# Optimization experiments

Measured on AMD Instinct MI355X. Metric: run time of the kernel, lower is better.

## Reference

```python
import jax, jax.numpy as jnp
import numpy as np

B, S, C = 16, 720, 862      # batch, seq_len, enc_in
P = 24                      # highest_freq_period
PAD = 720                   # seq_len % P == 0 -> pad_len == seq_len (no padding branch taken)
LQ = PAD // P               # 30, per-branch subsequence length == conv channels
DM = 128                    # d_model (PECBlock hidden conv channels)
EL = 2                      # e_layers
PRED = 336                  # pred_len
EPS = 1e-5                  # RevIN eps


def setup_inputs() -> dict:
    key = jax.random.key(0)
    ks = jax.random.split(key, 6)
    x = jax.random.normal(ks[0], (B, S, C), jnp.float32)
    # per-layer, per-branch pointwise conv weights (kernel_size=1, no bias)
    W1 = jax.random.normal(ks[1], (EL, P, DM, LQ), jnp.float32) * 0.05   # conv1: LQ -> DM
    W2 = jax.random.normal(ks[2], (EL, P, LQ, DM), jnp.float32) * 0.05   # conv2: DM -> LQ
    proj_w = jax.random.normal(ks[3], (PRED, S), jnp.float32) * 0.02      # Linear(seq_len, pred_len)
    proj_b = jnp.zeros((PRED,), jnp.float32)
    rev_w = jnp.ones((C,), jnp.float32)    # RevIN affine weight
    rev_b = jnp.zeros((C,), jnp.float32)   # RevIN affine bias
    return dict(x=x, W1=W1, W2=W2, proj_w=proj_w, proj_b=proj_b, rev_w=rev_w, rev_b=rev_b)


def reference(x, W1, W2, proj_w, proj_b, rev_w, rev_b):
    # RevIN 'norm': stats over time dim (unbiased=False var), affine
    mean = jnp.mean(x, axis=1, keepdims=True)
    stdev = jnp.sqrt(jnp.var(x, axis=1, keepdims=True) + EPS)
    xn = (x - mean) / stdev * rev_w + rev_b

    # seq_len % P == 0 so pad_time_series is identity
    x_padded = xn
    # NOTE: original loop feeds x_padded into EVERY block (not chained),
    # so each iteration overwrites y; replicated faithfully.
    # Strided gather idx::P == reshape (B,C,LQ,P) and index last axis;
    # scatter reassembly y[:,:,idx::P]=... == reshape back from (B,C,LQ,P).
    xs = x_padded.transpose(0, 2, 1).reshape(B, C, LQ, P)  # (B,C,LQ,P)
    y = x_padded
    for l in range(EL):
        h = jax.nn.gelu(jnp.einsum('pdq,bcqp->pbdc', W1[l], xs), approximate=False)  # (P,B,DM,C)
        ys = jnp.einsum('pqd,pbdc->bcqp', W2[l], h)                                  # (B,C,LQ,P)
        y = ys.reshape(B, C, PAD).transpose(0, 2, 1)                                 # (B,PAD,C)

    # PredictedProjection: Linear over time dim
    out = jnp.einsum('ps,bsc->bpc', proj_w, y[:, :S, :]) + proj_b[None, :, None]  # (B,PRED,C)

    # RevIN 'denorm'
    out = (out - rev_b) / (rev_w + EPS * EPS)
    out = out * stdev + mean
    return out
```

## Files before the change

kernel.cpp:

```cpp
#include <hip/hip_runtime.h>
#include <math.h>

typedef __attribute__((ext_vector_type(8))) short bf16x8;
typedef __attribute__((ext_vector_type(4))) short short4v;
typedef __attribute__((ext_vector_type(4))) float f32x4;

#define NB 16
#define NS 720
#define NC 862
#define NP 24
#define NQ 30
#define NDM 128
#define NPRED 336
#define BC (NB*NC)
#define SCH 10
#define SLEN 72
#define KP 768
#define PBASE (4*BC)
#define WOFF_F (24*BC)

__device__ __forceinline__ short f2bf(float f) {
    union { float f; unsigned u; } v; v.f = f;
    unsigned r = v.u + 0x7FFFu + ((v.u >> 16) & 1u);
    return (short)(r >> 16);
}

__device__ __forceinline__ float gelu_f(float h) {
    float hc = fminf(fmaxf(h, -8.f), 8.f);
    float z2 = hc * hc;
    float zz = hc * (0.79788456f + 0.035677408f * z2);
    float e  = __expf(-2.f * zz);
    return h * __builtin_amdgcn_rcpf(1.f + e);
}

__global__ __launch_bounds__(256) void stats_partial_k(const float* __restrict__ x,
                                                       float* __restrict__ ws) {
    int b = blockIdx.x, ct = blockIdx.y, ch = blockIdx.z;
    int c = ct * 256 + threadIdx.x;
    if (c >= NC) return;
    const float* xp = x + ((size_t)b * NS + (size_t)ch * SLEN) * NC + c;
    float s = 0.f, sq = 0.f;
    #pragma unroll 4
    for (int i = 0; i < SLEN; ++i) {
        float v = xp[(size_t)i * NC];
        s += v; sq += v * v;
    }
    int idx = b * NC + c;
    float* ps = ws + PBASE;
    ps[(size_t)ch * BC + idx] = s;
    ps[(size_t)(SCH + ch) * BC + idx] = sq;
}

__global__ __launch_bounds__(256) void stats_final_k(float* __restrict__ ws,
                                                     const float* __restrict__ revw,
                                                     const float* __restrict__ revb) {
    int idx = blockIdx.x * 256 + threadIdx.x;
    if (idx >= BC) return;
    const float* ps = ws + PBASE;
    float s = 0.f, sq = 0.f;
    #pragma unroll
    for (int ch = 0; ch < SCH; ++ch) {
        s  += ps[(size_t)ch * BC + idx];
        sq += ps[(size_t)(SCH + ch) * BC + idx];
    }
    int c = idx % NC;
    float mean  = s * (1.f / NS);
    float var   = sq * (1.f / NS) - mean * mean;
    float stdev = sqrtf(var + 1e-5f);
    float rstd  = 1.f / stdev;
    float aw = revw[c] * rstd;
    float u  = stdev / (revw[c] + 1e-10f);
    ws[idx]          = aw;
    ws[BC + idx]     = revb[c] - mean * aw;
    ws[2 * BC + idx] = u;
    ws[3 * BC + idx] = mean - revb[c] * u;
}

__global__ __launch_bounds__(256) void wprep_k(const float* __restrict__ W1,
                                               const float* __restrict__ W2,
                                               unsigned short* __restrict__ W1FF,
                                               unsigned short* __restrict__ W2FF) {
    int p = blockIdx.x, tid = threadIdx.x;
    const float* w1 = W1 + (size_t)(NP + p) * NDM * NQ;
    const float* w2 = W2 + (size_t)(NP + p) * NQ * NDM;
    #pragma unroll
    for (int pass = 0; pass < 2; ++pass) {
        int s = pass * 256 + tid;
        int l = s & 63, lr = l & 15, lg = l >> 4;
        {
            int dt = s >> 6;
            int d = dt * 16 + lr;
            bf16x8 v;
            #pragma unroll
            for (int j = 0; j < 8; ++j) {
                int q = 8 * lg + j;
                v[j] = f2bf(q < NQ ? w1[d * NQ + q] : 0.f);
            }
            ((bf16x8*)(W1FF + (size_t)p * 4096))[s] = v;
        }
        {
            int g = s >> 6, mi = g >> 2, ks = g & 3;
            int q = mi * 16 + lr, k = ks * 32 + 8 * lg;
            bf16x8 v;
            #pragma unroll
            for (int j = 0; j < 8; ++j)
                v[j] = f2bf(q < NQ ? w2[q * NDM + k + j] : 0.f);
            ((bf16x8*)(W2FF + (size_t)p * 4096))[s] = v;
        }
    }
}

__global__ __launch_bounds__(256) void pwprep_k(const float* __restrict__ pw,
                                                unsigned short* __restrict__ PWPF) {
    int t = blockIdx.x * 256 + threadIdx.x;
    if (t >= 24 * 24 * 64) return;
    int l = t & 63, ks = (t >> 6) % 24, st = t / (24 * 64);
    int lr = l & 15, lg = l >> 4;
    int m = st * 16 + lr;
    bf16x8 v;
    #pragma unroll
    for (int j = 0; j < 8; ++j) {
        int q = 8 * lg + j;
        v[j] = f2bf((m < NPRED && q < NQ) ? pw[(size_t)m * NS + q * NP + ks] : 0.f);
    }
    ((bf16x8*)PWPF)[t] = v;
}

__global__ __launch_bounds__(256) void branch_k(const float* __restrict__ x,
        const unsigned short* __restrict__ W1FF, const unsigned short* __restrict__ W2FF,
        const float* __restrict__ ws, unsigned short* __restrict__ y_t) {
    __shared__ __align__(16) short XsB[4 * 64 * 8];
    __shared__ __align__(16) short HB [16 * 64 * 8];
    int tid = threadIdx.x;
    int c0 = blockIdx.x * 64;
    int p  = blockIdx.y;
    int b  = blockIdx.z;

    {
        int c  = tid & 63, kb = tid >> 6;
        int cg = c0 + c;
        bool cv = cg < NC;
        int ce = cv ? cg : NC - 1;
        float aw = ws[b * NC + ce];
        float bw = ws[BC + b * NC + ce];
        const float* xb = x + ((size_t)b * NS + p) * NC + ce;
        bf16x8 v;
        #pragma unroll
        for (int j = 0; j < 8; ++j) {
            int q = kb * 8 + j;
            float val = (q < NQ && cv) ? xb[(size_t)q * NP * NC] * aw + bw : 0.f;
            v[j] = f2bf(val);
        }
        *(bf16x8*)&XsB[(size_t)(kb * 64 + (c ^ kb)) * 8] = v;
    }

    int w = tid >> 6, l = tid & 63, lr = l & 15, lg = l >> 4;
    f32x4 zf = {0.f, 0.f, 0.f, 0.f};
    const bf16x8* w1p = (const bf16x8*)(W1FF + (size_t)p * 4096);
    const bf16x8* w2p = (const bf16x8*)(W2FF + (size_t)p * 4096);
    bf16x8 a0 = w1p[(2 * w) * 64 + l];
    bf16x8 a1 = w1p[(2 * w + 1) * 64 + l];

    __syncthreads();

    f32x4 hc[2][4];
    #pragma unroll
    for (int ni = 0; ni < 4; ++ni) {
        bf16x8 bfr = *(const bf16x8*)&XsB[(size_t)(lg * 64 + ((ni * 16 + lr) ^ lg)) * 8];
        hc[0][ni] = __builtin_amdgcn_mfma_f32_16x16x32_bf16(a0, bfr, zf, 0, 0, 0);
        hc[1][ni] = __builtin_amdgcn_mfma_f32_16x16x32_bf16(a1, bfr, zf, 0, 0, 0);
    }
    #pragma unroll
    for (int mi2 = 0; mi2 < 2; ++mi2) {
        int d0 = (2 * w + mi2) * 16 + 4 * lg;
        int kb = d0 >> 3, sub = d0 & 7;
        #pragma unroll
        for (int ni = 0; ni < 4; ++ni) {
            short4v v;
            #pragma unroll
            for (int r = 0; r < 4; ++r)
                v[r] = f2bf(gelu_f(hc[mi2][ni][r]));
            int col = ni * 16 + lr;
            *(short4v*)&HB[(size_t)(kb * 64 + (col ^ kb)) * 8 + sub] = v;
        }
    }
    __syncthreads();

    f32x4 yacc[2] = {zf, zf};
    #pragma unroll
    for (int ks = 0; ks < 4; ++ks) {
        int kb = ks * 4 + lg;
        bf16x8 hfr = *(const bf16x8*)&HB[(size_t)(kb * 64 + ((w * 16 + lr) ^ kb)) * 8];
        #pragma unroll
        for (int mi = 0; mi < 2; ++mi) {
            bf16x8 w2f = w2p[(mi * 4 + ks) * 64 + l];
            yacc[mi] = __builtin_amdgcn_mfma_f32_16x16x32_bf16(w2f, hfr, yacc[mi], 0, 0, 0);
        }
    }
    int cg2 = c0 + w * 16 + lr;
    if (cg2 < NC) {
        unsigned short* base = y_t + ((size_t)(b * NC + cg2)) * KP + p * 32;
        #pragma unroll
        for (int mi = 0; mi < 2; ++mi) {
            int q0 = mi * 16 + 4 * lg;
            short4v v;
            #pragma unroll
            for (int r = 0; r < 4; ++r)
                v[r] = (q0 + r < NQ) ? f2bf(yacc[mi][r]) : (short)0;
            *(short4v*)(base + q0) = v;
        }
    }
}

__global__ __launch_bounds__(256) void proj_k(const unsigned short* __restrict__ PWPF,
        const float* __restrict__ pb, const float* __restrict__ ws,
        const unsigned short* __restrict__ y_t, float* __restrict__ out) {
    int tid = threadIdx.x;
    int n0 = blockIdx.x * 128, m0 = blockIdx.y * 64, b = blockIdx.z;
    int w = tid >> 6, l = tid & 63, lr = l & 15, lg = l >> 4;
    int st0 = m0 >> 4;
    f32x4 zf = {0.f, 0.f, 0.f, 0.f};
    f32x4 acc[4][2];
    #pragma unroll
    for (int mi = 0; mi < 4; ++mi) { acc[mi][0] = zf; acc[mi][1] = zf; }

    const unsigned short* ytb = y_t + (size_t)b * NC * KP;
    int cA = n0 + 2 * w * 16 + lr;        if (cA > NC - 1) cA = NC - 1;
    int cB = n0 + (2 * w + 1) * 16 + lr;  if (cB > NC - 1) cB = NC - 1;
    const unsigned short* rowA = ytb + (size_t)cA * KP + lg * 8;
    const unsigned short* rowB = ytb + (size_t)cB * KP + lg * 8;
    const bf16x8* apb = (const bf16x8*)PWPF + (size_t)st0 * 24 * 64 + l;

    union u16x8 { uint4 u; bf16x8 v; };
    bf16x8 af0[4], af1[4];
    u16x8 b00, b01, b10, b11;

#define LOADF(AF, B0, B1, KS) do {                                   \
        AF[0] = apb[(0 * 24 + (KS)) * 64];                           \
        AF[1] = apb[(1 * 24 + (KS)) * 64];                           \
        AF[2] = apb[(2 * 24 + (KS)) * 64];                           \
        AF[3] = apb[(3 * 24 + (KS)) * 64];                           \
        B0.u = *(const uint4*)(rowA + (KS) * 32);                    \
        B1.u = *(const uint4*)(rowB + (KS) * 32); } while (0)
#define MM(AF, B0, B1) do {                                          \
        _Pragma("unroll")                                            \
        for (int mi = 0; mi < 4; ++mi) {                             \
            acc[mi][0] = __builtin_amdgcn_mfma_f32_16x16x32_bf16(AF[mi], B0.v, acc[mi][0], 0, 0, 0); \
            acc[mi][1] = __builtin_amdgcn_mfma_f32_16x16x32_bf16(AF[mi], B1.v, acc[mi][1], 0, 0, 0); \
        } } while (0)

    LOADF(af0, b00, b01, 0);
    #pragma unroll
    for (int ks = 0; ks < 24; ks += 2) {
        LOADF(af1, b10, b11, ks + 1);
        MM(af0, b00, b01);
        if (ks + 2 < 24) LOADF(af0, b00, b01, ks + 2);
        MM(af1, b10, b11);
    }
#undef LOADF
#undef MM

    #pragma unroll
    for (int mi = 0; mi < 4; ++mi) {
        #pragma unroll
        for (int r = 0; r < 4; ++r) {
            int pr = m0 + mi * 16 + 4 * lg + r;
            if (pr >= NPRED) continue;
            float bias = pb[pr];
            #pragma unroll
            for (int nj = 0; nj < 2; ++nj) {
                int c = n0 + (2 * w + nj) * 16 + lr;
                if (c >= NC) continue;
                int idx = b * NC + c;
                out[((size_t)b * NPRED + pr) * NC + c] =
                    (acc[mi][nj][r] + bias) * ws[2 * BC + idx] + ws[3 * BC + idx];
            }
        }
    }
}

extern "C" void kernel_launch(void* const* d_in, const int* in_sizes, int n_in,
                              void* d_out, int out_size, void* d_ws, size_t ws_size,
                              hipStream_t stream) {
    const float* x   = (const float*)d_in[0];
    const float* W1  = (const float*)d_in[1];
    const float* W2  = (const float*)d_in[2];
    const float* pw  = (const float*)d_in[3];
    const float* pb  = (const float*)d_in[4];
    const float* rw  = (const float*)d_in[5];
    const float* rb  = (const float*)d_in[6];
    float* out = (float*)d_out;
    float* ws  = (float*)d_ws;
    unsigned short* W1FF = (unsigned short*)(ws + WOFF_F);
    unsigned short* W2FF = W1FF + NP * 4096;
    unsigned short* PWPF = W2FF + NP * 4096;
    unsigned short* y_t  = PWPF + 24 * 24 * 64 * 8;

    stats_partial_k<<<dim3(NB, 4, SCH), 256, 0, stream>>>(x, ws);
    wprep_k<<<dim3(NP), 256, 0, stream>>>(W1, W2, W1FF, W2FF);
    pwprep_k<<<dim3((24 * 24 * 64 + 255) / 256), 256, 0, stream>>>(pw, PWPF);
    stats_final_k<<<dim3((BC + 255) / 256), 256, 0, stream>>>(ws, rw, rb);
    branch_k<<<dim3(14, NP, NB), 256, 0, stream>>>(x, W1FF, W2FF, ws, y_t);
    proj_k<<<dim3(7, 6, NB), 256, 0, stream>>>(PWPF, pb, ws, y_t, out);
}
```

Measured before the change: 93.62 us.

## Stage projection operands through LDS with async global-to-LDS loads and flatten columns

Rewrites proj_k so each wave loads one A tile and two B tiles per k-step straight into double-buffered shared memory via global_load_lds. The waves then read all four A fragments from LDS, so the A fragments are shared across waves instead of every wave loading them from global memory. The batch and channel dimensions are flattened into one column axis, which removes the per-batch tail waste of partially filled 128-column tiles. A __syncthreads per k-step and an integer division in the epilogue are added in exchange.

```diff
diff --git a/kernel.cpp b/kernel.cpp
--- a/kernel.cpp
+++ b/kernel.cpp
@@ -18,6 +18,7 @@
 #define KP 768
 #define PBASE (4*BC)
 #define WOFF_F (24*BC)
+#define NCOL (NB*NC)
 
 __device__ __forceinline__ short f2bf(float f) {
     union { float f; unsigned u; } v; v.f = f;
@@ -31,6 +32,12 @@
     float zz = hc * (0.79788456f + 0.035677408f * z2);
     float e  = __expf(-2.f * zz);
     return h * __builtin_amdgcn_rcpf(1.f + e);
+}
+
+__device__ __forceinline__ void gl_lds16(const void* g, void* l) {
+    __builtin_amdgcn_global_load_lds(
+        (const __attribute__((address_space(1))) unsigned int*)g,
+        (__attribute__((address_space(3))) unsigned int*)l, 16, 0, 0);
 }
 
 __global__ __launch_bounds__(256) void stats_partial_k(const float* __restrict__ x,
@@ -212,53 +219,49 @@
     }
 }
 
-__global__ __launch_bounds__(256) void proj_k(const unsigned short* __restrict__ PWPF,
+__global__ __launch_bounds__(256, 4) void proj_k(const unsigned short* __restrict__ PWPF,
         const float* __restrict__ pb, const float* __restrict__ ws,
         const unsigned short* __restrict__ y_t, float* __restrict__ out) {
+    __shared__ __align__(16) short L[2][12 * 512];
     int tid = threadIdx.x;
-    int n0 = blockIdx.x * 128, m0 = blockIdx.y * 64, b = blockIdx.z;
     int w = tid >> 6, l = tid & 63, lr = l & 15, lg = l >> 4;
-    int st0 = m0 >> 4;
+    int gn0 = blockIdx.x * 128;
+    int m0  = blockIdx.y * 64;
     f32x4 zf = {0.f, 0.f, 0.f, 0.f};
     f32x4 acc[4][2];
     #pragma unroll
     for (int mi = 0; mi < 4; ++mi) { acc[mi][0] = zf; acc[mi][1] = zf; }
 
-    const unsigned short* ytb = y_t + (size_t)b * NC * KP;
-    int cA = n0 + 2 * w * 16 + lr;        if (cA > NC - 1) cA = NC - 1;
-    int cB = n0 + (2 * w + 1) * 16 + lr;  if (cB > NC - 1) cB = NC - 1;
-    const unsigned short* rowA = ytb + (size_t)cA * KP + lg * 8;
-    const unsigned short* rowB = ytb + (size_t)cB * KP + lg * 8;
-    const bf16x8* apb = (const bf16x8*)PWPF + (size_t)st0 * 24 * 64 + l;
-
-    union u16x8 { uint4 u; bf16x8 v; };
-    bf16x8 af0[4], af1[4];
-    u16x8 b00, b01, b10, b11;
-
-#define LOADF(AF, B0, B1, KS) do {                                   \
-        AF[0] = apb[(0 * 24 + (KS)) * 64];                           \
-        AF[1] = apb[(1 * 24 + (KS)) * 64];                           \
-        AF[2] = apb[(2 * 24 + (KS)) * 64];                           \
-        AF[3] = apb[(3 * 24 + (KS)) * 64];                           \
-        B0.u = *(const uint4*)(rowA + (KS) * 32);                    \
-        B1.u = *(const uint4*)(rowB + (KS) * 32); } while (0)
-#define MM(AF, B0, B1) do {                                          \
-        _Pragma("unroll")                                            \
-        for (int mi = 0; mi < 4; ++mi) {                             \
-            acc[mi][0] = __builtin_amdgcn_mfma_f32_16x16x32_bf16(AF[mi], B0.v, acc[mi][0], 0, 0, 0); \
-            acc[mi][1] = __builtin_amdgcn_mfma_f32_16x16x32_bf16(AF[mi], B1.v, acc[mi][1], 0, 0, 0); \
-        } } while (0)
-
-    LOADF(af0, b00, b01, 0);
-    #pragma unroll
-    for (int ks = 0; ks < 24; ks += 2) {
-        LOADF(af1, b10, b11, ks + 1);
-        MM(af0, b00, b01);
-        if (ks + 2 < 24) LOADF(af0, b00, b01, ks + 2);
-        MM(af1, b10, b11);
-    }
-#undef LOADF
-#undef MM
+    int cgA = gn0 + (2 * w) * 16 + lr;      if (cgA > NCOL - 1) cgA = NCOL - 1;
+    int cgB = gn0 + (2 * w + 1) * 16 + lr;  if (cgB > NCOL - 1) cgB = NCOL - 1;
+    const unsigned short* bsrcA = y_t + (size_t)cgA * KP + lg * 8;
+    const unsigned short* bsrcB = y_t + (size_t)cgB * KP + lg * 8;
+    const unsigned short* asrc  = PWPF + ((size_t)(m0 / 16 + w) * 24) * 512 + (size_t)l * 8;
+
+#define STAGE(BUF, KS) do {                                              \
+        gl_lds16(asrc  + (size_t)(KS) * 512, &L[BUF][w * 512]);          \
+        gl_lds16(bsrcA + (size_t)(KS) * 32,  &L[BUF][(4 + 2 * w) * 512]);\
+        gl_lds16(bsrcB + (size_t)(KS) * 32,  &L[BUF][(5 + 2 * w) * 512]);\
+    } while (0)
+
+    STAGE(0, 0);
+    __syncthreads();
+    int cur = 0;
+    for (int ks = 0; ks < 24; ++ks) {
+        if (ks + 1 < 24) STAGE(cur ^ 1, ks + 1);
+        const short* Lc = &L[cur][0];
+        bf16x8 b0 = *(const bf16x8*)&Lc[(4 + 2 * w) * 512 + l * 8];
+        bf16x8 b1 = *(const bf16x8*)&Lc[(5 + 2 * w) * 512 + l * 8];
+        #pragma unroll
+        for (int mi = 0; mi < 4; ++mi) {
+            bf16x8 a = *(const bf16x8*)&Lc[mi * 512 + l * 8];
+            acc[mi][0] = __builtin_amdgcn_mfma_f32_16x16x32_bf16(a, b0, acc[mi][0], 0, 0, 0);
+            acc[mi][1] = __builtin_amdgcn_mfma_f32_16x16x32_bf16(a, b1, acc[mi][1], 0, 0, 0);
+        }
+        __syncthreads();
+        cur ^= 1;
+    }
+#undef STAGE
 
     #pragma unroll
     for (int mi = 0; mi < 4; ++mi) {
@@ -269,11 +272,12 @@
             float bias = pb[pr];
             #pragma unroll
             for (int nj = 0; nj < 2; ++nj) {
-                int c = n0 + (2 * w + nj) * 16 + lr;
-                if (c >= NC) continue;
-                int idx = b * NC + c;
-                out[((size_t)b * NPRED + pr) * NC + c] =
-                    (acc[mi][nj][r] + bias) * ws[2 * BC + idx] + ws[3 * BC + idx];
+                int cg = gn0 + (2 * w + nj) * 16 + lr;
+                if (cg >= NCOL) continue;
+                int bb = cg / NC;
+                int cc = cg - bb * NC;
+                out[((size_t)bb * NPRED + pr) * NC + cc] =
+                    (acc[mi][nj][r] + bias) * ws[2 * BC + cg] + ws[3 * BC + cg];
             }
         }
     }
@@ -301,5 +305,5 @@
     pwprep_k<<<dim3((24 * 24 * 64 + 255) / 256), 256, 0, stream>>>(pw, PWPF);
     stats_final_k<<<dim3((BC + 255) / 256), 256, 0, stream>>>(ws, rw, rb);
     branch_k<<<dim3(14, NP, NB), 256, 0, stream>>>(x, W1FF, W2FF, ws, y_t);
-    proj_k<<<dim3(7, 6, NB), 256, 0, stream>>>(PWPF, pb, ws, y_t, out);
-}
+    proj_k<<<dim3((NCOL + 127) / 128, 6), 256, 0, stream>>>(PWPF, pb, ws, y_t, out);
+}
```

New measurement: 83.65 us. 1.12x faster.
